# Kernel tuning notes

Hardware: AMD Instinct MI355X
Metric: run time of the kernel (lower is better)

## Reference

```python
import jax, jax.numpy as jnp
import numpy as np

H = 512
INPUT_DIM = 13
OUTPUT_DIM = 1
W_DIM = (INPUT_DIM + OUTPUT_DIM) * H  # 7168
R = 256
N = 2048
LOG_2PI = float(np.log(2.0 * np.pi))


def setup_inputs() -> dict:
    key = jax.random.key(0)
    k1, k2, k3 = jax.random.split(key, 3)
    x = jax.random.normal(k1, (N, INPUT_DIM), dtype=jnp.float32)
    y = jax.random.normal(k2, (N, OUTPUT_DIM), dtype=jnp.float32)
    w = jax.random.normal(k3, (R, W_DIM), dtype=jnp.float32)
    return {"x": x, "y": y, "w": w}


def reference(x, y, w):
    # Batched version of FFReLU.loglik: for each weight sample r,
    #   w1 = w[r, :H*13].reshape(H, 13); w2 = w[r, H*13:].reshape(1, H)
    #   mu = w2 @ relu(w1 @ x.T)            -> [1, N]
    #   logprob[r] = Normal(mu.T, 1).log_prob(y).T
    w1_dim = H * INPUT_DIM
    w1 = w[:, :w1_dim].reshape(R, H, INPUT_DIM)       # [R, H, 13]
    w2 = w[:, w1_dim:].reshape(R, H)                  # [R, H] (output_dim = 1)
    hidden = jax.nn.relu(jnp.einsum('rhi,ni->rnh', w1, x))  # [R, N, H]
    mu = jnp.einsum('rnh,rh->rn', hidden, w2)         # [R, N]
    resid = y[:, 0][None, :] - mu                     # [R, N]
    log_p = -0.5 * resid * resid - 0.5 * LOG_2PI      # Normal(mu, 1) log-prob
    return log_p
```

## Files before the change

kernel.cpp:

```cpp
#include <hip/hip_runtime.h>

#define HH 512
#define IND 13
#define NN 2048
#define RR 256
#define WDIM 7168
#define W1DIM 6656
#define NBLK 256
#define NTHREADS 256
#define XPK_BYTES (NN * 32 * 2)
#define NEG_HALF_LOG_2PI (-0.91893853320467274f)

typedef __attribute__((ext_vector_type(8))) short short8;
typedef __attribute__((ext_vector_type(4))) float f32x4;
typedef __attribute__((ext_vector_type(2))) float f32x2;

__device__ __forceinline__ short f2bf(float f) {
    unsigned u = __float_as_uint(f);
    u += 0x7fffu + ((u >> 16) & 1u);
    return (short)(u >> 16);
}


__global__ __launch_bounds__(NTHREADS)
void xprep_kernel(const float* __restrict__ x, short* __restrict__ xpk) {
    const int n = blockIdx.x * NTHREADS + threadIdx.x;
    const float* xp = x + (size_t)n * IND;
    short tmp[32];
#pragma unroll
    for (int i = 0; i < 13; ++i) {
        float v = xp[i];
        unsigned u = __float_as_uint(v);
        tmp[i] = (short)(u >> 16);
        float res = v - __uint_as_float(u & 0xffff0000u);
        tmp[16 + i] = (short)(__float_as_uint(res) >> 16);
    }
    tmp[13] = 0; tmp[14] = 0; tmp[15] = 0;
    tmp[29] = 0; tmp[30] = 0; tmp[31] = 0;
    short8* dst = (short8*)(xpk + (size_t)n * 32);
    dst[0] = *(short8*)&tmp[0];
    dst[1] = *(short8*)&tmp[8];
    dst[2] = *(short8*)&tmp[16];
    dst[3] = *(short8*)&tmp[24];
}

template <bool FROM_WS>
__global__ __launch_bounds__(NTHREADS, 3)
void ffrelu_mfma_kernel(const float* __restrict__ x,
                        const float* __restrict__ y,
                        const float* __restrict__ w,
                        const short* __restrict__ xpk,
                        float* __restrict__ out) {
    __shared__ short Als[HH * 16];
    __shared__ float w2s[HH];

    const int tid = threadIdx.x;
    const int r = blockIdx.x;
    const int wave = tid >> 6;
    const int lane = tid & 63;
    const int m = lane & 15;
    const int q = lane >> 4;

    const float* wr = w + (size_t)r * WDIM;

#pragma unroll
    for (int rr = 0; rr < 2; ++rr) {
        const int h = tid * 2 + rr;
        const float* p = wr + (size_t)h * IND;
        short tmp[16];
#pragma unroll
        for (int i = 0; i < 13; ++i) tmp[i] = f2bf(p[i]);
        tmp[13] = 0; tmp[14] = 0; tmp[15] = 0;
        *(short8*)&Als[h * 16]     = *(short8*)&tmp[0];
        *(short8*)&Als[h * 16 + 8] = *(short8*)&tmp[8];
    }
    w2s[tid]       = wr[W1DIM + tid];
    w2s[tid + 256] = wr[W1DIM + tid + 256];
    __syncthreads();

    const bool lo  = (q >= 2);
    const bool hi8 = (q & 1);
    const f32x2 zero2 = {0.0f, 0.0f};
    const f32x4 czero = {0.0f, 0.0f, 0.0f, 0.0f};

    const int nb = blockIdx.y * NBLK + wave * 64;
    short8 bfrag[4];
    if (FROM_WS) {
        const short* base = xpk + (size_t)(nb + m) * 32 + (lo ? 16 : 0) + (hi8 ? 8 : 0);
#pragma unroll
        for (int nt = 0; nt < 4; ++nt) {
            bfrag[nt] = *(const short8*)(base + nt * 16 * 32);
        }
    } else {
#pragma unroll
        for (int nt = 0; nt < 4; ++nt) {
            const float* xp = x + (size_t)(nb + nt * 16 + m) * IND;
            short hs[13], ls[13];
#pragma unroll
            for (int i = 0; i < 13; ++i) {
                float v = xp[i];
                unsigned u = __float_as_uint(v);
                hs[i] = (short)(u >> 16);
                float res = v - __uint_as_float(u & 0xffff0000u);
                ls[i] = (short)(__float_as_uint(res) >> 16);
            }
            short s[13];
#pragma unroll
            for (int i = 0; i < 13; ++i) s[i] = lo ? ls[i] : hs[i];
            short8 b;
            b[0] = hi8 ? s[8]     : s[0];
            b[1] = hi8 ? s[9]     : s[1];
            b[2] = hi8 ? s[10]    : s[2];
            b[3] = hi8 ? s[11]    : s[3];
            b[4] = hi8 ? s[12]    : s[4];
            b[5] = hi8 ? (short)0 : s[5];
            b[6] = hi8 ? (short)0 : s[6];
            b[7] = hi8 ? (short)0 : s[7];
            bfrag[nt] = b;
        }
    }

    f32x2 muv[4][2];
#pragma unroll
    for (int i = 0; i < 4; ++i) {
        muv[i][0] = zero2;
        muv[i][1] = zero2;
    }

#pragma unroll 2
    for (int t = 0; t < 32; ++t) {
        const short8 a = *(const short8*)&Als[(t * 16 + m) * 16 + (q & 1) * 8];
        const f32x4 wv = *(const f32x4*)&w2s[t * 16 + q * 4];
        const f32x2 wv01 = {wv[0], wv[1]};
        const f32x2 wv23 = {wv[2], wv[3]};
#pragma unroll
        for (int nt = 0; nt < 4; ++nt) {
            f32x4 c = __builtin_amdgcn_mfma_f32_16x16x32_bf16(a, bfrag[nt], czero, 0, 0, 0);
            f32x2 c01 = {c[0], c[1]};
            f32x2 c23 = {c[2], c[3]};
            c01 = __builtin_elementwise_max(c01, zero2);
            c23 = __builtin_elementwise_max(c23, zero2);
            muv[nt][0] += c01 * wv01;
            muv[nt][1] += c23 * wv23;
        }
    }

    float mu[4];
#pragma unroll
    for (int nt = 0; nt < 4; ++nt) {
        f32x2 p = muv[nt][0] + muv[nt][1];
        float v = p[0] + p[1];
        v += __shfl_xor(v, 16, 64);
        v += __shfl_xor(v, 32, 64);
        mu[nt] = v;
    }

    float mu0;
    if (q == 0)      mu0 = mu[0];
    else if (q == 1) mu0 = mu[1];
    else if (q == 2) mu0 = mu[2];
    else             mu0 = mu[3];

    const int n0 = nb + lane;
    float resid0 = y[n0] - mu0;
    out[(size_t)r * NN + n0] = fmaf(-0.5f * resid0, resid0, NEG_HALF_LOG_2PI);
}

extern "C" void kernel_launch(void* const* d_in, const int* in_sizes, int n_in,
                              void* d_out, int out_size, void* d_ws, size_t ws_size,
                              hipStream_t stream) {
    const float* x = (const float*)d_in[0];
    const float* y = (const float*)d_in[1];
    const float* w = (const float*)d_in[2];
    float* out = (float*)d_out;
    short* xpk = (short*)d_ws;

    dim3 grid(RR, NN / NBLK);
    dim3 block(NTHREADS);

    if (ws_size >= (size_t)XPK_BYTES) {
        xprep_kernel<<<NN / NTHREADS, NTHREADS, 0, stream>>>(x, xpk);
        ffrelu_mfma_kernel<true><<<grid, block, 0, stream>>>(x, y, w, xpk, out);
    } else {
        ffrelu_mfma_kernel<false><<<grid, block, 0, stream>>>(x, y, w, xpk, out);
    }
}
```

Measured before the change: 91.27 us.

## Split hidden dimension across wave pairs with 8 N-tiles per wave

Each wave now covers 128 samples (8 N-tiles) over half of the hidden units instead of 64 samples over all hidden units. Partial mu values are reduced across the two hidden halves through LDS, and the y loads are hoisted ahead of the barrier. Each A fragment loaded from LDS now feeds twice as many MFMAs, cutting LDS read traffic, and the occupancy hint rises to 4 blocks. The cost is more registers for 8 B fragments and accumulators, plus two extra barriers and an LDS reduction at the end.

```diff
diff --git a/kernel.cpp b/kernel.cpp
--- a/kernel.cpp
+++ b/kernel.cpp
@@ -7,6 +7,7 @@
 #define WDIM 7168
 #define W1DIM 6656
 #define NBLK 256
+#define NT 8
 #define NTHREADS 256
 #define XPK_BYTES (NN * 32 * 2)
 #define NEG_HALF_LOG_2PI (-0.91893853320467274f)
@@ -45,7 +46,7 @@
 }
 
 template <bool FROM_WS>
-__global__ __launch_bounds__(NTHREADS, 3)
+__global__ __launch_bounds__(NTHREADS, 4)
 void ffrelu_mfma_kernel(const float* __restrict__ x,
                         const float* __restrict__ y,
                         const float* __restrict__ w,
@@ -60,6 +61,8 @@
     const int lane = tid & 63;
     const int m = lane & 15;
     const int q = lane >> 4;
+    const int hseg = wave >> 1;
+    const int npart = wave & 1;
 
     const float* wr = w + (size_t)r * WDIM;
 
@@ -76,24 +79,23 @@
     }
     w2s[tid]       = wr[W1DIM + tid];
     w2s[tid + 256] = wr[W1DIM + tid + 256];
-    __syncthreads();
 
     const bool lo  = (q >= 2);
     const bool hi8 = (q & 1);
     const f32x2 zero2 = {0.0f, 0.0f};
     const f32x4 czero = {0.0f, 0.0f, 0.0f, 0.0f};
 
-    const int nb = blockIdx.y * NBLK + wave * 64;
-    short8 bfrag[4];
+    const int nb = blockIdx.y * NBLK + npart * 128;
+    short8 bfrag[NT];
     if (FROM_WS) {
         const short* base = xpk + (size_t)(nb + m) * 32 + (lo ? 16 : 0) + (hi8 ? 8 : 0);
 #pragma unroll
-        for (int nt = 0; nt < 4; ++nt) {
+        for (int nt = 0; nt < NT; ++nt) {
             bfrag[nt] = *(const short8*)(base + nt * 16 * 32);
         }
     } else {
 #pragma unroll
-        for (int nt = 0; nt < 4; ++nt) {
+        for (int nt = 0; nt < NT; ++nt) {
             const float* xp = x + (size_t)(nb + nt * 16 + m) * IND;
             short hs[13], ls[13];
 #pragma unroll
@@ -120,21 +122,28 @@
         }
     }
 
-    f32x2 muv[4][2];
-#pragma unroll
-    for (int i = 0; i < 4; ++i) {
+    const float yv0 = y[nb + lane];
+    const float yv1 = y[nb + 64 + lane];
+
+    __syncthreads();
+
+    f32x2 muv[NT][2];
+#pragma unroll
+    for (int i = 0; i < NT; ++i) {
         muv[i][0] = zero2;
         muv[i][1] = zero2;
     }
 
+    const int tbase = hseg * 16;
 #pragma unroll 2
-    for (int t = 0; t < 32; ++t) {
-        const short8 a = *(const short8*)&Als[(t * 16 + m) * 16 + (q & 1) * 8];
-        const f32x4 wv = *(const f32x4*)&w2s[t * 16 + q * 4];
+    for (int t = 0; t < 16; ++t) {
+        const int tg = tbase + t;
+        const short8 a = *(const short8*)&Als[(tg * 16 + m) * 16 + (q & 1) * 8];
+        const f32x4 wv = *(const f32x4*)&w2s[tg * 16 + q * 4];
         const f32x2 wv01 = {wv[0], wv[1]};
         const f32x2 wv23 = {wv[2], wv[3]};
 #pragma unroll
-        for (int nt = 0; nt < 4; ++nt) {
+        for (int nt = 0; nt < NT; ++nt) {
             f32x4 c = __builtin_amdgcn_mfma_f32_16x16x32_bf16(a, bfrag[nt], czero, 0, 0, 0);
             f32x2 c01 = {c[0], c[1]};
             f32x2 c23 = {c[2], c[3]};
@@ -145,9 +154,9 @@
         }
     }
 
-    float mu[4];
-#pragma unroll
-    for (int nt = 0; nt < 4; ++nt) {
+    float mu[NT];
+#pragma unroll
+    for (int nt = 0; nt < NT; ++nt) {
         f32x2 p = muv[nt][0] + muv[nt][1];
         float v = p[0] + p[1];
         v += __shfl_xor(v, 16, 64);
@@ -155,15 +164,29 @@
         mu[nt] = v;
     }
 
-    float mu0;
-    if (q == 0)      mu0 = mu[0];
-    else if (q == 1) mu0 = mu[1];
-    else if (q == 2) mu0 = mu[2];
-    else             mu0 = mu[3];
-
-    const int n0 = nb + lane;
-    float resid0 = y[n0] - mu0;
-    out[(size_t)r * NN + n0] = fmaf(-0.5f * resid0, resid0, NEG_HALF_LOG_2PI);
+    float mu0, mu1;
+    if (q == 0)      { mu0 = mu[0]; mu1 = mu[4]; }
+    else if (q == 1) { mu0 = mu[1]; mu1 = mu[5]; }
+    else if (q == 2) { mu0 = mu[2]; mu1 = mu[6]; }
+    else             { mu0 = mu[3]; mu1 = mu[7]; }
+
+    float* mubuf = (float*)Als;
+    __syncthreads();
+    if (hseg == 1) {
+        mubuf[npart * 128 + lane]       = mu0;
+        mubuf[256 + npart * 128 + lane] = mu1;
+    }
+    __syncthreads();
+    if (hseg == 0) {
+        mu0 += mubuf[npart * 128 + lane];
+        mu1 += mubuf[256 + npart * 128 + lane];
+        const int n0 = nb + lane;
+        float resid0 = yv0 - mu0;
+        float resid1 = yv1 - mu1;
+        float* op = out + (size_t)r * NN;
+        op[n0]      = fmaf(-0.5f * resid0, resid0, NEG_HALF_LOG_2PI);
+        op[n0 + 64] = fmaf(-0.5f * resid1, resid1, NEG_HALF_LOG_2PI);
+    }
 }
 
 extern "C" void kernel_launch(void* const* d_in, const int* in_sizes, int n_in,
```

After: 93.26 us. 1.02x slower.

## Pre-pack W1/W2 to bf16 in workspace and load via global_load_lds

Applied to the files above, without the earlier changes.

A combined prep kernel now converts w1 to padded bf16 rows and copies w2 into workspace once, alongside the x packing. The main kernel then fills its LDS tiles with direct global-to-LDS DMA instead of each of the 8 N-blocks per r redoing strided fp32 loads and conversions. The y load is hoisted before the barrier. In exchange it adds a larger workspace requirement and an extra pass over all of w in the prep kernel, and the fast path depends on ws_size being large enough.

```diff
diff --git a/kernel.cpp b/kernel.cpp
--- a/kernel.cpp
+++ b/kernel.cpp
@@ -7,9 +7,16 @@
 #define WDIM 7168
 #define W1DIM 6656
 #define NBLK 256
+#define NT 4
 #define NTHREADS 256
-#define XPK_BYTES (NN * 32 * 2)
 #define NEG_HALF_LOG_2PI (-0.91893853320467274f)
+
+#define XPK_BYTES   (NN * 32 * 2)
+#define W1PK_OFF    XPK_BYTES
+#define W1PK_BYTES  (RR * HH * 16 * 2)
+#define W2PK_OFF    (W1PK_OFF + W1PK_BYTES)
+#define W2PK_BYTES  (RR * HH * 4)
+#define WS_NEEDED   (W2PK_OFF + W2PK_BYTES)
 
 typedef __attribute__((ext_vector_type(8))) short short8;
 typedef __attribute__((ext_vector_type(4))) float f32x4;
@@ -21,27 +28,51 @@
     return (short)(u >> 16);
 }
 
+#define GLDS16(gsrc, ldst) \
+    __builtin_amdgcn_global_load_lds( \
+        (const __attribute__((address_space(1))) void*)(gsrc), \
+        (__attribute__((address_space(3))) void*)(ldst), 16, 0, 0)
+
 
 __global__ __launch_bounds__(NTHREADS)
-void xprep_kernel(const float* __restrict__ x, short* __restrict__ xpk) {
-    const int n = blockIdx.x * NTHREADS + threadIdx.x;
-    const float* xp = x + (size_t)n * IND;
-    short tmp[32];
-#pragma unroll
-    for (int i = 0; i < 13; ++i) {
-        float v = xp[i];
-        unsigned u = __float_as_uint(v);
-        tmp[i] = (short)(u >> 16);
-        float res = v - __uint_as_float(u & 0xffff0000u);
-        tmp[16 + i] = (short)(__float_as_uint(res) >> 16);
-    }
-    tmp[13] = 0; tmp[14] = 0; tmp[15] = 0;
-    tmp[29] = 0; tmp[30] = 0; tmp[31] = 0;
-    short8* dst = (short8*)(xpk + (size_t)n * 32);
-    dst[0] = *(short8*)&tmp[0];
-    dst[1] = *(short8*)&tmp[8];
-    dst[2] = *(short8*)&tmp[16];
-    dst[3] = *(short8*)&tmp[24];
+void prep_kernel(const float* __restrict__ x, const float* __restrict__ w,
+                 short* __restrict__ xpk, short* __restrict__ w1pk,
+                 float* __restrict__ w2pk) {
+    const int b = blockIdx.x;
+    const int tid = threadIdx.x;
+    if (b < 512) {
+        const int gid = b * NTHREADS + tid;
+        const int r = gid >> 9;
+        const int h = gid & 511;
+        const float* p = w + (size_t)r * WDIM + (size_t)h * IND;
+        short tmp[16];
+#pragma unroll
+        for (int i = 0; i < 13; ++i) tmp[i] = f2bf(p[i]);
+        tmp[13] = 0; tmp[14] = 0; tmp[15] = 0;
+        short8* dst = (short8*)(w1pk + (size_t)gid * 16);
+        dst[0] = *(short8*)&tmp[0];
+        dst[1] = *(short8*)&tmp[8];
+        w2pk[gid] = w[(size_t)r * WDIM + W1DIM + h];
+    } else {
+        const int n = (b - 512) * NTHREADS + tid;
+        const float* xp = x + (size_t)n * IND;
+        short tmp[32];
+#pragma unroll
+        for (int i = 0; i < 13; ++i) {
+            float v = xp[i];
+            unsigned u = __float_as_uint(v);
+            tmp[i] = (short)(u >> 16);
+            float res = v - __uint_as_float(u & 0xffff0000u);
+            tmp[16 + i] = (short)(__float_as_uint(res) >> 16);
+        }
+        tmp[13] = 0; tmp[14] = 0; tmp[15] = 0;
+        tmp[29] = 0; tmp[30] = 0; tmp[31] = 0;
+        short8* dst = (short8*)(xpk + (size_t)n * 32);
+        dst[0] = *(short8*)&tmp[0];
+        dst[1] = *(short8*)&tmp[8];
+        dst[2] = *(short8*)&tmp[16];
+        dst[3] = *(short8*)&tmp[24];
+    }
 }
 
 template <bool FROM_WS>
@@ -50,6 +81,8 @@
                         const float* __restrict__ y,
                         const float* __restrict__ w,
                         const short* __restrict__ xpk,
+                        const short* __restrict__ w1pk,
+                        const float* __restrict__ w2pk,
                         float* __restrict__ out) {
     __shared__ short Als[HH * 16];
     __shared__ float w2s[HH];
@@ -61,22 +94,33 @@
     const int m = lane & 15;
     const int q = lane >> 4;
 
-    const float* wr = w + (size_t)r * WDIM;
-
-#pragma unroll
-    for (int rr = 0; rr < 2; ++rr) {
-        const int h = tid * 2 + rr;
-        const float* p = wr + (size_t)h * IND;
-        short tmp[16];
-#pragma unroll
-        for (int i = 0; i < 13; ++i) tmp[i] = f2bf(p[i]);
-        tmp[13] = 0; tmp[14] = 0; tmp[15] = 0;
-        *(short8*)&Als[h * 16]     = *(short8*)&tmp[0];
-        *(short8*)&Als[h * 16 + 8] = *(short8*)&tmp[8];
-    }
-    w2s[tid]       = wr[W1DIM + tid];
-    w2s[tid + 256] = wr[W1DIM + tid + 256];
-    __syncthreads();
+    if (FROM_WS) {
+        const char* w1g = (const char*)(w1pk + (size_t)r * (HH * 16))
+                          + wave * 4096 + (size_t)lane * 16;
+        char* alsb = (char*)Als + wave * 4096;
+#pragma unroll
+        for (int i = 0; i < 4; ++i) GLDS16(w1g + i * 1024, alsb + i * 1024);
+        if (wave < 2) {
+            const char* w2g = (const char*)(w2pk + (size_t)r * HH)
+                              + wave * 1024 + (size_t)lane * 16;
+            GLDS16(w2g, (char*)w2s + wave * 1024);
+        }
+    } else {
+        const float* wr = w + (size_t)r * WDIM;
+#pragma unroll
+        for (int rr = 0; rr < 2; ++rr) {
+            const int h = tid * 2 + rr;
+            const float* p = wr + (size_t)h * IND;
+            short tmp[16];
+#pragma unroll
+            for (int i = 0; i < 13; ++i) tmp[i] = f2bf(p[i]);
+            tmp[13] = 0; tmp[14] = 0; tmp[15] = 0;
+            *(short8*)&Als[h * 16]     = *(short8*)&tmp[0];
+            *(short8*)&Als[h * 16 + 8] = *(short8*)&tmp[8];
+        }
+        w2s[tid]       = wr[W1DIM + tid];
+        w2s[tid + 256] = wr[W1DIM + tid + 256];
+    }
 
     const bool lo  = (q >= 2);
     const bool hi8 = (q & 1);
@@ -84,16 +128,16 @@
     const f32x4 czero = {0.0f, 0.0f, 0.0f, 0.0f};
 
     const int nb = blockIdx.y * NBLK + wave * 64;
-    short8 bfrag[4];
+    short8 bfrag[NT];
     if (FROM_WS) {
         const short* base = xpk + (size_t)(nb + m) * 32 + (lo ? 16 : 0) + (hi8 ? 8 : 0);
 #pragma unroll
-        for (int nt = 0; nt < 4; ++nt) {
+        for (int nt = 0; nt < NT; ++nt) {
             bfrag[nt] = *(const short8*)(base + nt * 16 * 32);
         }
     } else {
 #pragma unroll
-        for (int nt = 0; nt < 4; ++nt) {
+        for (int nt = 0; nt < NT; ++nt) {
             const float* xp = x + (size_t)(nb + nt * 16 + m) * IND;
             short hs[13], ls[13];
 #pragma unroll
@@ -120,9 +164,13 @@
         }
     }
 
-    f32x2 muv[4][2];
-#pragma unroll
-    for (int i = 0; i < 4; ++i) {
+    const float yv = y[nb + lane];
+
+    __syncthreads();
+
+    f32x2 muv[NT][2];
+#pragma unroll
+    for (int i = 0; i < NT; ++i) {
         muv[i][0] = zero2;
         muv[i][1] = zero2;
     }
@@ -134,7 +182,7 @@
         const f32x2 wv01 = {wv[0], wv[1]};
         const f32x2 wv23 = {wv[2], wv[3]};
 #pragma unroll
-        for (int nt = 0; nt < 4; ++nt) {
+        for (int nt = 0; nt < NT; ++nt) {
             f32x4 c = __builtin_amdgcn_mfma_f32_16x16x32_bf16(a, bfrag[nt], czero, 0, 0, 0);
             f32x2 c01 = {c[0], c[1]};
             f32x2 c23 = {c[2], c[3]};
@@ -145,9 +193,9 @@
         }
     }
 
-    float mu[4];
-#pragma unroll
-    for (int nt = 0; nt < 4; ++nt) {
+    float mu[NT];
+#pragma unroll
+    for (int nt = 0; nt < NT; ++nt) {
         f32x2 p = muv[nt][0] + muv[nt][1];
         float v = p[0] + p[1];
         v += __shfl_xor(v, 16, 64);
@@ -162,7 +210,7 @@
     else             mu0 = mu[3];
 
     const int n0 = nb + lane;
-    float resid0 = y[n0] - mu0;
+    float resid0 = yv - mu0;
     out[(size_t)r * NN + n0] = fmaf(-0.5f * resid0, resid0, NEG_HALF_LOG_2PI);
 }
 
@@ -173,15 +221,18 @@
     const float* y = (const float*)d_in[1];
     const float* w = (const float*)d_in[2];
     float* out = (float*)d_out;
-    short* xpk = (short*)d_ws;
+    char* ws = (char*)d_ws;
+    short* xpk  = (short*)ws;
+    short* w1pk = (short*)(ws + W1PK_OFF);
+    float* w2pk = (float*)(ws + W2PK_OFF);
 
     dim3 grid(RR, NN / NBLK);
     dim3 block(NTHREADS);
 
-    if (ws_size >= (size_t)XPK_BYTES) {
-        xprep_kernel<<<NN / NTHREADS, NTHREADS, 0, stream>>>(x, xpk);
-        ffrelu_mfma_kernel<true><<<grid, block, 0, stream>>>(x, y, w, xpk, out);
-    } else {
-        ffrelu_mfma_kernel<false><<<grid, block, 0, stream>>>(x, y, w, xpk, out);
-    }
-}
+    if (ws_size >= (size_t)WS_NEEDED) {
+        prep_kernel<<<520, NTHREADS, 0, stream>>>(x, w, xpk, w1pk, w2pk);
+        ffrelu_mfma_kernel<true><<<grid, block, 0, stream>>>(x, y, w, xpk, w1pk, w2pk, out);
+    } else {
+        ffrelu_mfma_kernel<false><<<grid, block, 0, stream>>>(x, y, w, xpk, w1pk, w2pk, out);
+    }
+}
```

New measurement: 91.65 us. No clear change (+0.4%).
